# Optimization experiments

Hardware: AMD Instinct MI355X
Metric: run time of the kernel (lower is better)

The kernel has to match this reference:

```python
import jax, jax.numpy as jnp
import numpy as np
from jax import lax

DIM = 256
NUM_HEADS = 8
SW = 7
HEAD_DIM = DIM // NUM_HEADS
SCALE = HEAD_DIM ** -0.5


def setup_inputs() -> dict:
    key = jax.random.key(0)
    ks = jax.random.split(key, 7)
    B, C, H, W = 8, DIM, 56, 56
    x = jax.random.normal(ks[0], (B, C, H, W), dtype=jnp.float32)
    w_qkv = jax.random.normal(ks[1], (3 * C, C), dtype=jnp.float32) * 0.02
    b_qkv = jnp.zeros((3 * C,), dtype=jnp.float32)
    # depthwise 3x3 kernel, OIHW with feature_group_count=C -> (C,1,3,3)
    w_dw = jax.random.normal(ks[2], (C, 1, 3, 3), dtype=jnp.float32) * 0.02
    b_dw = jnp.zeros((C,), dtype=jnp.float32)
    w_proj = jax.random.normal(ks[3], (C, C), dtype=jnp.float32) * 0.02
    b_proj = jnp.zeros((C,), dtype=jnp.float32)
    return {"x": x, "w_qkv": w_qkv, "b_qkv": b_qkv, "w_dw": w_dw,
            "b_dw": b_dw, "w_proj": w_proj, "b_proj": b_proj}


def _conv1x1(x, w, b):
    # x:[B,C,H,W], w:[O,C] -> [B,O,H,W]
    return jnp.einsum('bchw,oc->bohw', x, w) + b[None, :, None, None]


def _dwconv3x3(x, w, b):
    C = x.shape[1]
    y = lax.conv_general_dilated(x, w, window_strides=(1, 1), padding='SAME',
                                 dimension_numbers=('NCHW', 'OIHW', 'NCHW'),
                                 feature_group_count=C)
    return y + b[None, :, None, None]


def _stripe_attn_H(q, k, v, sw):
    # q,k,v: [B,h,C,H,W]; local attention within sw-thick horizontal stripes
    B, h, C, H, W = q.shape
    sw = min(sw, H)
    pad = (-H) % sw
    if pad:
        pw = [(0, 0)] * 3 + [(0, pad), (0, 0)]
        q = jnp.pad(q, pw); k = jnp.pad(k, pw); v = jnp.pad(v, pw)
    Hp = H + pad
    n = Hp // sw

    def rs(t):
        # -> [B,h,n, sw*W, C]
        return t.reshape(B, h, C, n, sw, W).transpose(0, 1, 3, 4, 5, 2).reshape(B, h, n, sw * W, C)

    qs, ks_, vs = rs(q) * SCALE, rs(k), rs(v)
    attn = jax.nn.softmax(jnp.einsum('bhnqc,bhnkc->bhnqk', qs, ks_), axis=-1)
    out = jnp.einsum('bhnqk,bhnkc->bhnqc', attn, vs)
    out = out.reshape(B, h, n, sw, W, C).transpose(0, 1, 5, 2, 3, 4).reshape(B, h, C, Hp, W)
    return out[:, :, :, :H, :]


def _stripe_attn_W(q, k, v, sw):
    # attention within sw-thick vertical stripes; softmax is permutation-
    # equivariant over the stripe sequence, so transposing H<->W and reusing
    # the H-stripe kernel computes identical math.
    t = lambda a: a.transpose(0, 1, 2, 4, 3)
    return t(_stripe_attn_H(t(q), t(k), t(v), sw))


def reference(x, w_qkv, b_qkv, w_dw, b_dw, w_proj, b_proj):
    B, C, H, W = x.shape
    hh = NUM_HEADS // 2
    qkv = _conv1x1(x, w_qkv, b_qkv)
    q, k, v = jnp.split(qkv, 3, axis=1)
    v = v + _dwconv3x3(v, w_dw, b_dw)

    def heads(t):
        return t.reshape(B, NUM_HEADS, HEAD_DIM, H, W)

    q, k, v = heads(q), heads(k), heads(v)
    out_h = _stripe_attn_H(q[:, :hh], k[:, :hh], v[:, :hh], SW)
    out_w = _stripe_attn_W(q[:, hh:], k[:, hh:], v[:, hh:], SW)
    out = jnp.concatenate([out_h, out_w], axis=1).reshape(B, C, H, W)
    return _conv1x1(out, w_proj, b_proj)
```

## Files before the change

### kernel.cpp

```cpp
#include <hip/hip_runtime.h>
#include <hip/hip_bf16.h>
#include <stdint.h>

#define Bn 8
#define Cn 256
#define Hn 56
#define Wn 56
#define HWn 3136
#define NHEADS 8
#define HDIM 32
#define SEQ 392
#define SEQP 400
#define NSTR 8
#define QKV_LD 768
#define KSC (0.17677669529663689f * 1.4426950408889634f)

#if __has_builtin(__builtin_amdgcn_exp2f)
#define EXP2(x) __builtin_amdgcn_exp2f(x)
#else
#define EXP2(x) exp2f(x)
#endif

typedef short short8 __attribute__((ext_vector_type(8)));
typedef float floatx4 __attribute__((ext_vector_type(4)));

__device__ __forceinline__ unsigned short f2bf(float f) {
  union { float f; uint32_t u; } v; v.f = f;
  uint32_t u = v.u;
  u += 0x7fffu + ((u >> 16) & 1u);
  return (unsigned short)(u >> 16);
}
__device__ __forceinline__ float bf2f(unsigned short h) {
  union { uint32_t u; float f; } v; v.u = ((uint32_t)h) << 16;
  return v.f;
}
__device__ __forceinline__ uint32_t cvt_pk_bf16(float lo, float hi) {
  uint32_t r;
  asm("v_cvt_pk_bf16_f32 %0, %1, %2" : "=v"(r) : "v"(lo), "v"(hi));
  return r;
}

__global__ __launch_bounds__(256) void k_cvt2(const float* __restrict__ a,
                                              const float* __restrict__ b2,
                                              unsigned short* __restrict__ da,
                                              unsigned short* __restrict__ db) {
  int i = blockIdx.x * 256 + threadIdx.x;
  if (i < 49152) {
    float4 v = ((const float4*)a)[i];
    ushort4 o;
    o.x = f2bf(v.x); o.y = f2bf(v.y); o.z = f2bf(v.z); o.w = f2bf(v.w);
    ((ushort4*)da)[i] = o;
  } else {
    int k = i - 49152;
    float4 v = ((const float4*)b2)[k];
    ushort4 o;
    o.x = f2bf(v.x); o.y = f2bf(v.y); o.z = f2bf(v.z); o.w = f2bf(v.w);
    ((ushort4*)db)[k] = o;
  }
}

__global__ __launch_bounds__(256) void k_trans_x(const float* __restrict__ x,
                                                 unsigned short* __restrict__ xt) {
  __shared__ float tile[32][33];
  int pb = blockIdx.x, cb = blockIdx.y, b = blockIdx.z;
  int t = threadIdx.x;
  int c = t >> 3, p4 = (t & 7) * 4;
  float4 v = *(const float4*)(x + (((size_t)b * Cn + cb * 32 + c) * HWn + pb * 32 + p4));
  tile[c][p4 + 0] = v.x; tile[c][p4 + 1] = v.y; tile[c][p4 + 2] = v.z; tile[c][p4 + 3] = v.w;
  __syncthreads();
  int p = t >> 3, c4 = (t & 7) * 4;
  ushort4 o;
  o.x = f2bf(tile[c4 + 0][p]); o.y = f2bf(tile[c4 + 1][p]);
  o.z = f2bf(tile[c4 + 2][p]); o.w = f2bf(tile[c4 + 3][p]);
  *(ushort4*)(xt + (((size_t)b * HWn + pb * 32 + p) * Cn + cb * 32 + c4)) = o;
}

template <int EPI>
__global__ __launch_bounds__(256) void k_gemm(const unsigned short* __restrict__ A,
                                              const unsigned short* __restrict__ Bt,
                                              const float* __restrict__ bias,
                                              unsigned short* __restrict__ outB,
                                              float* __restrict__ outF,
                                              int M, int N, int K) {
  __shared__ __align__(16) unsigned short As[128 * 72];
  __shared__ __align__(16) unsigned short Bs[128 * 72];
  int t = threadIdx.x;
  int n0 = blockIdx.x * 128, m0 = blockIdx.y * 128;
  int b = blockIdx.z;
  const unsigned short* Bb = Bt + (size_t)b * N * K;
  int lane = t & 63, w = t >> 6;
  int wr = w >> 1, wc = w & 1;
  int g = lane >> 4, q = lane & 15;

  floatx4 z4 = {0.f, 0.f, 0.f, 0.f};
  floatx4 acc[4][4];
#pragma unroll
  for (int i = 0; i < 4; i++)
#pragma unroll
    for (int j = 0; j < 4; j++) acc[i][j] = z4;

  for (int k0 = 0; k0 < K; k0 += 64) {
    short8 ra[4], rb[4];
#pragma unroll
    for (int i = 0; i < 4; i++) {
      int j = i * 256 + t;
      int row = j >> 3, col = (j & 7) * 8;
      ra[i] = *(const short8*)(A + (size_t)(m0 + row) * K + k0 + col);
      int nr = n0 + row;
      if (nr < N) {
        rb[i] = *(const short8*)(Bb + (size_t)nr * K + k0 + col);
      } else {
        short8 z = {0, 0, 0, 0, 0, 0, 0, 0};
        rb[i] = z;
      }
    }
    __syncthreads();
#pragma unroll
    for (int i = 0; i < 4; i++) {
      int j = i * 256 + t;
      int row = j >> 3, col = (j & 7) * 8;
      *(short8*)&As[row * 72 + col] = ra[i];
      *(short8*)&Bs[row * 72 + col] = rb[i];
    }
    __syncthreads();
#pragma unroll
    for (int kk = 0; kk < 64; kk += 32) {
      short8 af[4], bfr[4];
#pragma unroll
      for (int i = 0; i < 4; i++)
        af[i] = *(const short8*)&As[(wr * 64 + i * 16 + q) * 72 + kk + g * 8];
#pragma unroll
      for (int j = 0; j < 4; j++)
        bfr[j] = *(const short8*)&Bs[(wc * 64 + j * 16 + q) * 72 + kk + g * 8];
#pragma unroll
      for (int i = 0; i < 4; i++)
#pragma unroll
        for (int j = 0; j < 4; j++)
          acc[i][j] = __builtin_amdgcn_mfma_f32_16x16x32_bf16(af[i], bfr[j], acc[i][j], 0, 0, 0);
    }
    __syncthreads();
  }

#pragma unroll
  for (int i = 0; i < 4; i++) {
    int ob = m0 + wr * 64 + i * 16 + g * 4;
    float bs0 = bias[ob + 0], bs1 = bias[ob + 1], bs2 = bias[ob + 2], bs3 = bias[ob + 3];
    float sc = 1.0f;
    if (EPI == 0 && ob >= 256 && ob < 512) sc = KSC;
#pragma unroll
    for (int j = 0; j < 4; j++) {
      int col = n0 + wc * 64 + j * 16 + q;
      if (col < N) {
        if (EPI == 0) {
          ushort4 o;
          o.x = f2bf((acc[i][j][0] + bs0) * sc);
          o.y = f2bf((acc[i][j][1] + bs1) * sc);
          o.z = f2bf((acc[i][j][2] + bs2) * sc);
          o.w = f2bf((acc[i][j][3] + bs3) * sc);
          *(ushort4*)(outB + ((size_t)b * N + col) * M + ob) = o;
        } else {
          float* po = outF + (size_t)b * M * N;
          po[(size_t)(ob + 0) * N + col] = acc[i][j][0] + bs0;
          po[(size_t)(ob + 1) * N + col] = acc[i][j][1] + bs1;
          po[(size_t)(ob + 2) * N + col] = acc[i][j][2] + bs2;
          po[(size_t)(ob + 3) * N + col] = acc[i][j][3] + bs3;
        }
      }
    }
  }
}

__global__ __launch_bounds__(256) void k_dwconv_t(const unsigned short* __restrict__ qkv,
                                                  const float* __restrict__ wdw,
                                                  const float* __restrict__ bdw,
                                                  unsigned short* __restrict__ vmt) {
  __shared__ float wS[1152];
  __shared__ float bS[128];
  __shared__ __align__(16) unsigned short tile[16][140];
  int t = threadIdx.x;
  int pass = blockIdx.y, b = blockIdx.z;
  for (int i = t; i < 1152; i += 256) wS[i] = wdw[pass * 1152 + i];
  if (t < 128) bS[t] = bdw[pass * 128 + t];
  __syncthreads();

  int pi = t >> 4, c8 = (t & 15) * 8;
  int i16 = blockIdx.x * 16 + pi;
  int h, w;
  if (pass == 0) { h = i16 / Wn; w = i16 % Wn; }
  else           { w = i16 / Hn; h = i16 % Hn; }

  const unsigned short* vq = qkv + 512 + pass * 128 + c8;
  float a[8];
  short8 vc = *(const short8*)(vq + ((size_t)b * HWn + h * Wn + w) * QKV_LD);
#pragma unroll
  for (int e = 0; e < 8; e++) a[e] = bf2f((unsigned short)vc[e]) + bS[c8 + e];
#pragma unroll
  for (int ky = 0; ky < 3; ky++) {
    int hh = h + ky - 1;
    if (hh < 0 || hh >= Hn) continue;
#pragma unroll
    for (int kx = 0; kx < 3; kx++) {
      int ww = w + kx - 1;
      if (ww < 0 || ww >= Wn) continue;
      short8 vn = *(const short8*)(vq + ((size_t)b * HWn + hh * Wn + ww) * QKV_LD);
#pragma unroll
      for (int e = 0; e < 8; e++) a[e] += bf2f((unsigned short)vn[e]) * wS[(c8 + e) * 9 + ky * 3 + kx];
    }
  }
  short8 o;
#pragma unroll
  for (int e = 0; e < 8; e++) o[e] = (short)f2bf(a[e]);
  *(short8*)&tile[pi][c8] = o;
  __syncthreads();

  int dd = t >> 1, half = t & 1;
  short8 ov;
#pragma unroll
  for (int k2 = 0; k2 < 8; k2++) ov[k2] = (short)tile[half * 8 + k2][dd];
  *(short8*)(vmt + ((size_t)(b * Cn + pass * 128 + dd)) * HWn + blockIdx.x * 16 + half * 8) = ov;
}

__global__ __launch_bounds__(256) void k_attn(const unsigned short* __restrict__ qkv,
                                              const unsigned short* __restrict__ vmt,
                                              unsigned short* __restrict__ aout) {
  __shared__ __align__(16) unsigned short Ks[12288];
  __shared__ __align__(16) unsigned short Vf[12800];
  __shared__ __align__(16) unsigned short Pf[2048];
  int s = blockIdx.x;
  int hd = blockIdx.y & 7, b = blockIdx.y >> 3;
  int part = blockIdx.z;
  int t = threadIdx.x, lane = t & 63, wv = t >> 6;
  bool wst = (hd >= 4);
  int q = lane & 15, g = lane >> 4;

  const unsigned short* kg = qkv + 256 + hd * HDIM;
#pragma unroll
  for (int P = 0; P < 6; P++) {
    int key = P * 64 + wv * 16 + q;
    int gg = (t >> 4) & 3;
    int p = wst ? ((key % Wn) * Wn + s * 7 + key / Wn) : (s * SEQ + key);
    short8 kv = *(const short8*)(kg + (size_t)(b * HWn + p) * QKV_LD + gg * 8);
    *(short8*)&Ks[((((key >> 4) * 4 + gg) * 16) + (key & 15)) * 8] = kv;
  }
  short8 kf24;
  {
    int key = 384 + q; if (key > 391) key = 391;
    int p = wst ? ((key % Wn) * Wn + s * 7 + key / Wn) : (s * SEQ + key);
    kf24 = *(const short8*)(kg + (size_t)(b * HWn + p) * QKV_LD + g * 8);
  }
  const unsigned short* vg = vmt + ((size_t)(b * Cn + hd * HDIM)) * HWn + s * SEQ;
  for (int idx = t; idx < 1600; idx += 256) {
    int d = idx / 50, Gc = idx % 50;
    short8 vv = *(const short8*)(vg + (size_t)d * HWn + Gc * 8);
    *(short8*)&Vf[(Gc * 32 + (d ^ (Gc & 7))) * 8] = vv;
  }
  __syncthreads();

  floatx4 z4 = {0.f, 0.f, 0.f, 0.f};
  unsigned short* Pw = &Pf[wv * 512];
  int gh = g >> 1, ge = (g & 1) * 4;

  int qb0 = part * 13, qb1 = part ? 25 : 13;
  for (int qb = qb0 + wv; qb < qb1; qb += 4) {
    int qi = qb * 16 + q;
    int qil = (qi < SEQ) ? qi : 0;
    int pq = wst ? ((qil % Wn) * Wn + s * 7 + qil / Wn) : (s * SEQ + qil);
    short8 qf = *(const short8*)(qkv + ((size_t)b * HWn + pq) * QKV_LD + hd * HDIM + g * 8);

    floatx4 sacc[25];
#pragma unroll
    for (int j = 0; j < 24; j++) {
      short8 kf = *(const short8*)&Ks[((j * 4 + g) * 16 + q) * 8];
      sacc[j] = __builtin_amdgcn_mfma_f32_16x16x32_bf16(kf, qf, z4, 0, 0, 0);
    }
    sacc[24] = __builtin_amdgcn_mfma_f32_16x16x32_bf16(kf24, qf, z4, 0, 0, 0);
    if (g >= 2) { sacc[24][0] = sacc[24][1] = sacc[24][2] = sacc[24][3] = -3.0e38f; }

    float sm = 0.f;
#pragma unroll
    for (int j = 0; j < 25; j++) {
      float e0 = EXP2(sacc[j][0]); float e1 = EXP2(sacc[j][1]);
      float e2 = EXP2(sacc[j][2]); float e3 = EXP2(sacc[j][3]);
      sacc[j][0] = e0; sacc[j][1] = e1; sacc[j][2] = e2; sacc[j][3] = e3;
      sm += (e0 + e1) + (e2 + e3);
    }
    sm += __shfl_xor(sm, 16);
    sm += __shfl_xor(sm, 32);
    float rcp = 1.0f / sm;

#define WRITEP(cc) do {                                                        \
    uint2 wA, wB;                                                              \
    wA.x = cvt_pk_bf16(sacc[2*(cc)][0], sacc[2*(cc)][1]);                      \
    wA.y = cvt_pk_bf16(sacc[2*(cc)][2], sacc[2*(cc)][3]);                      \
    if (2*(cc)+1 < 25) {                                                       \
      wB.x = cvt_pk_bf16(sacc[2*(cc)+1][0], sacc[2*(cc)+1][1]);                \
      wB.y = cvt_pk_bf16(sacc[2*(cc)+1][2], sacc[2*(cc)+1][3]);                \
    } else { wB.x = 0u; wB.y = 0u; }                                           \
    *(uint2*)&Pw[(gh * 16 + q) * 8 + ge] = wA;                                 \
    *(uint2*)&Pw[((2 + gh) * 16 + q) * 8 + ge] = wB;                           \
  } while (0)

    floatx4 o0 = z4, o1 = z4;
    WRITEP(0);
#pragma unroll
    for (int ch = 0; ch < 13; ch++) {
      asm volatile("s_waitcnt lgkmcnt(0)" ::: "memory");
      short8 pfr = *(const short8*)&Pw[(g * 16 + q) * 8];
      int Gc = ch * 4 + g; if (Gc > 49) Gc = 49;
      int sw = Gc & 7;
      short8 vf0 = *(const short8*)&Vf[(Gc * 32 + (q ^ sw)) * 8];
      short8 vf1 = *(const short8*)&Vf[(Gc * 32 + 16 + (q ^ sw)) * 8];
      if (ch < 12) {
        switch (ch + 1) {
          case 1: WRITEP(1); break;  case 2: WRITEP(2); break;
          case 3: WRITEP(3); break;  case 4: WRITEP(4); break;
          case 5: WRITEP(5); break;  case 6: WRITEP(6); break;
          case 7: WRITEP(7); break;  case 8: WRITEP(8); break;
          case 9: WRITEP(9); break;  case 10: WRITEP(10); break;
          case 11: WRITEP(11); break; case 12: WRITEP(12); break;
        }
      }
      o0 = __builtin_amdgcn_mfma_f32_16x16x32_bf16(vf0, pfr, o0, 0, 0, 0);
      o1 = __builtin_amdgcn_mfma_f32_16x16x32_bf16(vf1, pfr, o1, 0, 0, 0);
    }
#undef WRITEP

    if (qi < SEQ) {
      size_t ob = ((size_t)b * HWn + pq) * Cn + hd * HDIM;
      ushort4 u0, u1;
      u0.x = f2bf(o0[0] * rcp); u0.y = f2bf(o0[1] * rcp);
      u0.z = f2bf(o0[2] * rcp); u0.w = f2bf(o0[3] * rcp);
      u1.x = f2bf(o1[0] * rcp); u1.y = f2bf(o1[1] * rcp);
      u1.z = f2bf(o1[2] * rcp); u1.w = f2bf(o1[3] * rcp);
      *(ushort4*)(aout + ob + g * 4) = u0;
      *(ushort4*)(aout + ob + 16 + g * 4) = u1;
    }
  }
}

extern "C" void kernel_launch(void* const* d_in, const int* in_sizes, int n_in,
                              void* d_out, int out_size, void* d_ws, size_t ws_size,
                              hipStream_t stream) {
  const float* x     = (const float*)d_in[0];
  const float* wqkv  = (const float*)d_in[1];
  const float* bqkv  = (const float*)d_in[2];
  const float* wdw   = (const float*)d_in[3];
  const float* bdw   = (const float*)d_in[4];
  const float* wproj = (const float*)d_in[5];
  const float* bproj = (const float*)d_in[6];
  float* out = (float*)d_out;

  unsigned short* xt   = (unsigned short*)d_ws;
  unsigned short* wqb  = xt + (size_t)Bn * HWn * Cn;
  unsigned short* wpb  = wqb + 768 * 256;
  unsigned short* qkvb = wpb + 256 * 256;
  unsigned short* vmt  = qkvb + (size_t)Bn * HWn * QKV_LD;
  unsigned short* aout = vmt + (size_t)Bn * HWn * Cn;

  k_cvt2<<<dim3(256), 256, 0, stream>>>(wqkv, wproj, wqb, wpb);
  k_trans_x<<<dim3(98, 8, Bn), 256, 0, stream>>>(x, xt);
  k_gemm<0><<<dim3(25, 6, Bn), 256, 0, stream>>>(wqb, xt, bqkv, qkvb, nullptr, 768, HWn, 256);
  k_dwconv_t<<<dim3(196, 2, Bn), 256, 0, stream>>>(qkvb, wdw, bdw, vmt);
  k_attn<<<dim3(NSTR, Bn * NHEADS, 2), 256, 0, stream>>>(qkvb, vmt, aout);
  k_gemm<1><<<dim3(25, 2, Bn), 256, 0, stream>>>(wpb, aout, bproj, nullptr, out, 256, HWn, 256);
}
```

Measured before the change: 117.4 us.

## Use async global-to-LDS loads with XOR swizzle and write transposed Q/K copy

```diff
diff --git a/kernel.cpp b/kernel.cpp
--- a/kernel.cpp
+++ b/kernel.cpp
@@ -10,7 +10,6 @@
 #define NHEADS 8
 #define HDIM 32
 #define SEQ 392
-#define SEQP 400
 #define NSTR 8
 #define QKV_LD 768
 #define KSC (0.17677669529663689f * 1.4426950408889634f)
@@ -38,6 +37,10 @@
   uint32_t r;
   asm("v_cvt_pk_bf16_f32 %0, %1, %2" : "=v"(r) : "v"(lo), "v"(hi));
   return r;
+}
+__device__ __forceinline__ void gload16(const unsigned short* g, unsigned short* l) {
+  __builtin_amdgcn_global_load_lds((const __attribute__((address_space(1))) void*)g,
+                                   (__attribute__((address_space(3))) void*)l, 16, 0, 0);
 }
 
 __global__ __launch_bounds__(256) void k_cvt2(const float* __restrict__ a,
@@ -81,9 +84,10 @@
                                               const float* __restrict__ bias,
                                               unsigned short* __restrict__ outB,
                                               float* __restrict__ outF,
+                                              unsigned short* __restrict__ qkvw,
                                               int M, int N, int K) {
-  __shared__ __align__(16) unsigned short As[128 * 72];
-  __shared__ __align__(16) unsigned short Bs[128 * 72];
+  __shared__ __align__(16) unsigned short As[128 * 64];
+  __shared__ __align__(16) unsigned short Bs[128 * 64];
   int t = threadIdx.x;
   int n0 = blockIdx.x * 128, m0 = blockIdx.y * 128;
   int b = blockIdx.z;
@@ -91,6 +95,8 @@
   int lane = t & 63, w = t >> 6;
   int wr = w >> 1, wc = w & 1;
   int g = lane >> 4, q = lane & 15;
+  int srow = w * 32 + (lane >> 3);
+  int slot = lane & 7;
 
   floatx4 z4 = {0.f, 0.f, 0.f, 0.f};
   floatx4 acc[4][4];
@@ -100,45 +106,42 @@
     for (int j = 0; j < 4; j++) acc[i][j] = z4;
 
   for (int k0 = 0; k0 < K; k0 += 64) {
-    short8 ra[4], rb[4];
+    __syncthreads();
 #pragma unroll
     for (int i = 0; i < 4; i++) {
-      int j = i * 256 + t;
-      int row = j >> 3, col = (j & 7) * 8;
-      ra[i] = *(const short8*)(A + (size_t)(m0 + row) * K + k0 + col);
+      int row = srow + i * 8;
+      int cs = slot ^ (row & 7);
+      gload16(A + (size_t)(m0 + row) * K + k0 + cs * 8, &As[(w * 32 + i * 8) * 64]);
+    }
+#pragma unroll
+    for (int i = 0; i < 4; i++) {
+      int row = srow + i * 8;
+      int cs = slot ^ (row & 7);
       int nr = n0 + row;
-      if (nr < N) {
-        rb[i] = *(const short8*)(Bb + (size_t)nr * K + k0 + col);
-      } else {
-        short8 z = {0, 0, 0, 0, 0, 0, 0, 0};
-        rb[i] = z;
-      }
-    }
-    __syncthreads();
-#pragma unroll
-    for (int i = 0; i < 4; i++) {
-      int j = i * 256 + t;
-      int row = j >> 3, col = (j & 7) * 8;
-      *(short8*)&As[row * 72 + col] = ra[i];
-      *(short8*)&Bs[row * 72 + col] = rb[i];
-    }
+      if (nr < N)
+        gload16(Bb + (size_t)nr * K + k0 + cs * 8, &Bs[(w * 32 + i * 8) * 64]);
+    }
+    asm volatile("s_waitcnt vmcnt(0)" ::: "memory");
     __syncthreads();
 #pragma unroll
     for (int kk = 0; kk < 64; kk += 32) {
       short8 af[4], bfr[4];
 #pragma unroll
-      for (int i = 0; i < 4; i++)
-        af[i] = *(const short8*)&As[(wr * 64 + i * 16 + q) * 72 + kk + g * 8];
-#pragma unroll
-      for (int j = 0; j < 4; j++)
-        bfr[j] = *(const short8*)&Bs[(wc * 64 + j * 16 + q) * 72 + kk + g * 8];
+      for (int i = 0; i < 4; i++) {
+        int row = wr * 64 + i * 16 + q;
+        af[i] = *(const short8*)&As[row * 64 + ((((kk >> 3) + g) ^ (q & 7)) << 3)];
+      }
+#pragma unroll
+      for (int j = 0; j < 4; j++) {
+        int row = wc * 64 + j * 16 + q;
+        bfr[j] = *(const short8*)&Bs[row * 64 + ((((kk >> 3) + g) ^ (q & 7)) << 3)];
+      }
 #pragma unroll
       for (int i = 0; i < 4; i++)
 #pragma unroll
         for (int j = 0; j < 4; j++)
           acc[i][j] = __builtin_amdgcn_mfma_f32_16x16x32_bf16(af[i], bfr[j], acc[i][j], 0, 0, 0);
     }
-    __syncthreads();
   }
 
 #pragma unroll
@@ -158,6 +161,13 @@
           o.z = f2bf((acc[i][j][2] + bs2) * sc);
           o.w = f2bf((acc[i][j][3] + bs3) * sc);
           *(ushort4*)(outB + ((size_t)b * N + col) * M + ob) = o;
+          int wch = -1;
+          if (ob >= 128 && ob < 256) wch = ob - 128;
+          else if (ob >= 384 && ob < 512) wch = ob - 384 + 128;
+          if (wch >= 0) {
+            int pw = (col % Wn) * Wn + col / Wn;
+            *(ushort4*)(qkvw + ((size_t)b * HWn + pw) * 256 + wch) = o;
+          }
         } else {
           float* po = outF + (size_t)b * M * N;
           po[(size_t)(ob + 0) * N + col] = acc[i][j][0] + bs0;
@@ -221,6 +231,7 @@
 }
 
 __global__ __launch_bounds__(256) void k_attn(const unsigned short* __restrict__ qkv,
+                                              const unsigned short* __restrict__ qkvw,
                                               const unsigned short* __restrict__ vmt,
                                               unsigned short* __restrict__ aout) {
   __shared__ __align__(16) unsigned short Ks[12288];
@@ -232,23 +243,37 @@
   int t = threadIdx.x, lane = t & 63, wv = t >> 6;
   bool wst = (hd >= 4);
   int q = lane & 15, g = lane >> 4;
-
-  const unsigned short* kg = qkv + 256 + hd * HDIM;
+  int sbase = s * SEQ;
+
+  const unsigned short* base; int ld, qoff, koff;
+  if (wst) { base = qkvw + (size_t)b * HWn * 256;    ld = 256;    qoff = (hd - 4) * 32; koff = 128 + (hd - 4) * 32; }
+  else     { base = qkv  + (size_t)b * HWn * QKV_LD; ld = QKV_LD; qoff = hd * 32;       koff = 256 + hd * 32; }
+
+  int qb0 = part * 13, qb1 = part ? 25 : 13;
+
+  short8 qpre[4];
+#pragma unroll
+  for (int it = 0; it < 4; it++) {
+    int qb = qb0 + wv + it * 4;
+    int qi = qb * 16 + q;
+    int qil = (qi < SEQ) ? qi : 391;
+    qpre[it] = *(const short8*)(base + qoff + (size_t)(sbase + qil) * ld + g * 8);
+  }
+
+  const unsigned short* kgp = base + koff;
 #pragma unroll
   for (int P = 0; P < 6; P++) {
     int key = P * 64 + wv * 16 + q;
     int gg = (t >> 4) & 3;
-    int p = wst ? ((key % Wn) * Wn + s * 7 + key / Wn) : (s * SEQ + key);
-    short8 kv = *(const short8*)(kg + (size_t)(b * HWn + p) * QKV_LD + gg * 8);
+    short8 kv = *(const short8*)(kgp + (size_t)(sbase + key) * ld + gg * 8);
     *(short8*)&Ks[((((key >> 4) * 4 + gg) * 16) + (key & 15)) * 8] = kv;
   }
   short8 kf24;
   {
     int key = 384 + q; if (key > 391) key = 391;
-    int p = wst ? ((key % Wn) * Wn + s * 7 + key / Wn) : (s * SEQ + key);
-    kf24 = *(const short8*)(kg + (size_t)(b * HWn + p) * QKV_LD + g * 8);
-  }
-  const unsigned short* vg = vmt + ((size_t)(b * Cn + hd * HDIM)) * HWn + s * SEQ;
+    kf24 = *(const short8*)(kgp + (size_t)(sbase + key) * ld + g * 8);
+  }
+  const unsigned short* vg = vmt + ((size_t)(b * Cn + hd * HDIM)) * HWn + sbase;
   for (int idx = t; idx < 1600; idx += 256) {
     int d = idx / 50, Gc = idx % 50;
     short8 vv = *(const short8*)(vg + (size_t)d * HWn + Gc * 8);
@@ -260,12 +285,13 @@
   unsigned short* Pw = &Pf[wv * 512];
   int gh = g >> 1, ge = (g & 1) * 4;
 
-  int qb0 = part * 13, qb1 = part ? 25 : 13;
-  for (int qb = qb0 + wv; qb < qb1; qb += 4) {
+#pragma unroll
+  for (int it = 0; it < 4; it++) {
+    int qb = qb0 + wv + it * 4;
+    if (qb >= qb1) continue;
     int qi = qb * 16 + q;
-    int qil = (qi < SEQ) ? qi : 0;
-    int pq = wst ? ((qil % Wn) * Wn + s * 7 + qil / Wn) : (s * SEQ + qil);
-    short8 qf = *(const short8*)(qkv + ((size_t)b * HWn + pq) * QKV_LD + hd * HDIM + g * 8);
+    int qil = (qi < SEQ) ? qi : 391;
+    short8 qf = qpre[it];
 
     floatx4 sacc[25];
 #pragma unroll
@@ -326,6 +352,7 @@
 #undef WRITEP
 
     if (qi < SEQ) {
+      int pq = wst ? ((qil % Wn) * Wn + s * 7 + qil / Wn) : (sbase + qil);
       size_t ob = ((size_t)b * HWn + pq) * Cn + hd * HDIM;
       ushort4 u0, u1;
       u0.x = f2bf(o0[0] * rcp); u0.y = f2bf(o0[1] * rcp);
@@ -356,11 +383,12 @@
   unsigned short* qkvb = wpb + 256 * 256;
   unsigned short* vmt  = qkvb + (size_t)Bn * HWn * QKV_LD;
   unsigned short* aout = vmt + (size_t)Bn * HWn * Cn;
+  unsigned short* qkvw = aout + (size_t)Bn * HWn * Cn;
 
   k_cvt2<<<dim3(256), 256, 0, stream>>>(wqkv, wproj, wqb, wpb);
   k_trans_x<<<dim3(98, 8, Bn), 256, 0, stream>>>(x, xt);
-  k_gemm<0><<<dim3(25, 6, Bn), 256, 0, stream>>>(wqb, xt, bqkv, qkvb, nullptr, 768, HWn, 256);
+  k_gemm<0><<<dim3(25, 6, Bn), 256, 0, stream>>>(wqb, xt, bqkv, qkvb, nullptr, qkvw, 768, HWn, 256);
   k_dwconv_t<<<dim3(196, 2, Bn), 256, 0, stream>>>(qkvb, wdw, bdw, vmt);
-  k_attn<<<dim3(NSTR, Bn * NHEADS, 2), 256, 0, stream>>>(qkvb, vmt, aout);
-  k_gemm<1><<<dim3(25, 2, Bn), 256, 0, stream>>>(wpb, aout, bproj, nullptr, out, 256, HWn, 256);
-}
+  k_attn<<<dim3(NSTR, Bn * NHEADS, 2), 256, 0, stream>>>(qkvb, qkvw, vmt, aout);
+  k_gemm<1><<<dim3(25, 2, Bn), 256, 0, stream>>>(wpb, aout, bproj, nullptr, out, nullptr, 256, HWn, 256);
+}
```

Result: no change. 118.3 us (+0.8%).
